# Optimization experiments

Hardware: AMD Instinct MI355X
Metric: run time of the kernel (lower is better)

The kernel has to match this reference:

```python
import jax, jax.numpy as jnp
import numpy as np

HEADS = 4
DIM_HEAD = 32
SCALE = DIM_HEAD ** (-0.5)


def setup_inputs() -> dict:
    key = jax.random.key(0)
    k0, k1, k2 = jax.random.split(key, 3)
    B, C, H, W = 4, 256, 64, 64
    inner = HEADS * DIM_HEAD  # 128
    x = jax.random.normal(k0, (B, C, H, W), dtype=jnp.float32)
    # 1x1 conv weights reduce to matrices (out_ch, in_ch)
    w_qkv = jax.random.normal(k1, (3 * inner, C), dtype=jnp.float32) * 0.02
    w_out = jax.random.normal(k2, (C, inner), dtype=jnp.float32) * 0.02
    b_out = jnp.zeros((C,), dtype=jnp.float32)
    return {"x": x, "w_qkv": w_qkv, "w_out": w_out, "b_out": b_out}


def reference(x, w_qkv, w_out, b_out):
    b, c, h, w = x.shape
    n = h * w  # flattened spatial length
    inner = HEADS * DIM_HEAD
    # 1x1 conv == channel matmul: [b, 3*inner, h, w]
    qkv = jnp.einsum('oc,bchw->bohw', w_qkv, x)
    qkv = qkv.reshape(b, 3, HEADS, DIM_HEAD, n)  # split 3 * (heads dim_head)
    q, k, v = qkv[:, 0], qkv[:, 1], qkv[:, 2]    # each [b, heads, d, n]
    sim = jnp.einsum('bhdi,bhdj->bhij', q * SCALE, k)  # [b, h, n, n]
    attn = jax.nn.softmax(sim, axis=-1)  # stable (max-subtract) softmax
    out = jnp.einsum('bhij,bhdj->bhid', attn, v)       # [b, heads, n, d]
    # 'b h (x y) d -> b (h d) x y'
    out = out.transpose(0, 1, 3, 2).reshape(b, inner, h, w)
    y = jnp.einsum('oc,bchw->bohw', w_out, out) + b_out[None, :, None, None]
    return y
```

## Files before the change

kernel.cpp:

```cpp
#include <hip/hip_runtime.h>

#define N_TOK 4096
#define BATCH 4

typedef __attribute__((ext_vector_type(8))) short short8;
typedef __attribute__((ext_vector_type(4))) float floatx4;

__device__ __forceinline__ unsigned pack_rnd(float a, float b) {
    unsigned ra = __float_as_uint(a) + 0x8000u;
    unsigned rb = __float_as_uint(b) + 0x8000u;
    return __builtin_amdgcn_perm(rb, ra, 0x07060302u);
}

__device__ __forceinline__ void split_pack(float a, float b,
                                           unsigned &ph, unsigned &pl) {
    unsigned ra = __float_as_uint(a) + 0x8000u;
    unsigned rb = __float_as_uint(b) + 0x8000u;
    ph = __builtin_amdgcn_perm(rb, ra, 0x07060302u);
    float la = a - __uint_as_float(ra & 0xffff0000u);
    float lb = b - __uint_as_float(rb & 0xffff0000u);
    pl = __builtin_amdgcn_perm(__float_as_uint(lb) + 0x8000u,
                               __float_as_uint(la) + 0x8000u, 0x07060302u);
}

__device__ __forceinline__ short8 mk_short8(unsigned p0, unsigned p1,
                                            unsigned p2, unsigned p3) {
    union { unsigned u[4]; short8 s; } c;
    c.u[0] = p0; c.u[1] = p1; c.u[2] = p2; c.u[3] = p3;
    return c.s;
}

__device__ __forceinline__ void cvt_frag(const float* src,
                                         short8 &hi, short8 &lo) {
    float4 w0 = *(const float4*)src;
    float4 w1 = *(const float4*)(src + 4);
    unsigned ph[4], pl[4];
    split_pack(w0.x, w0.y, ph[0], pl[0]);
    split_pack(w0.z, w0.w, ph[1], pl[1]);
    split_pack(w1.x, w1.y, ph[2], pl[2]);
    split_pack(w1.z, w1.w, ph[3], pl[3]);
    hi = mk_short8(ph[0], ph[1], ph[2], ph[3]);
    lo = mk_short8(pl[0], pl[1], pl[2], pl[3]);
}

__device__ __forceinline__ float fast_exp2(float x) {
#if __has_builtin(__builtin_amdgcn_exp2f)
    return __builtin_amdgcn_exp2f(x);
#else
    return exp2f(x);
#endif
}

__global__ __launch_bounds__(256) void gemm1_fused(
    const float* __restrict__ wq, const float* __restrict__ x,
    unsigned short* __restrict__ Qp, unsigned short* __restrict__ Kp,
    unsigned short* __restrict__ Vp)
{
    const int N = N_TOK;
    const int b = blockIdx.z;
    const int row0 = blockIdx.y * 64;
    const int col0 = blockIdx.x * 64;
    const int t = threadIdx.x;
    const int wave = t >> 6, lane = t & 63;
    const int l16 = lane & 15, quad = lane >> 4;
    const int msub0 = (wave & 1) * 32, nsub0 = (wave >> 1) * 32;

    __shared__ __align__(16) char smem[29184];
    float (*Xf)[68] = (float(*)[68])smem;
    unsigned short* XsH = (unsigned short*)(smem + 8704);
    unsigned short* XsL = (unsigned short*)(smem + 13824);
    unsigned short* WsH = (unsigned short*)(smem + 18944);
    unsigned short* WsL = (unsigned short*)(smem + 24064);

    floatx4 acc[2][2] = {};

    const int xr = t >> 3, xnb = (t & 7) * 8;
    const int tnr = t >> 2, tkb = (t & 3) * 8;
    const int wm = t >> 2, wk = (t & 3) * 8;

    for (int kc = 0; kc < 8; ++kc) {
        __syncthreads();
        {
            const float* wsrc = wq + (size_t)(row0 + wm) * 256 + kc * 32 + wk;
            float4 w0 = *(const float4*)wsrc;
            float4 w1 = *(const float4*)(wsrc + 4);
            unsigned ph[4], pl[4];
            split_pack(w0.x, w0.y, ph[0], pl[0]);
            split_pack(w0.z, w0.w, ph[1], pl[1]);
            split_pack(w1.x, w1.y, ph[2], pl[2]);
            split_pack(w1.z, w1.w, ph[3], pl[3]);
            *(uint4*)(WsH + wm * 40 + wk) = *(uint4*)ph;
            *(uint4*)(WsL + wm * 40 + wk) = *(uint4*)pl;
        }
        {
            const float* src = x + ((size_t)b * 256 + kc * 32 + xr) * N + col0 + xnb;
            *(float4*)&Xf[xr][xnb]     = *(const float4*)src;
            *(float4*)&Xf[xr][xnb + 4] = *(const float4*)(src + 4);
        }
        __syncthreads();
        {
            unsigned ph[4], pl[4];
#pragma unroll
            for (int q = 0; q < 4; ++q)
                split_pack(Xf[tkb + 2 * q][tnr], Xf[tkb + 2 * q + 1][tnr],
                           ph[q], pl[q]);
            *(uint4*)(XsH + tnr * 40 + tkb) = *(uint4*)ph;
            *(uint4*)(XsL + tnr * 40 + tkb) = *(uint4*)pl;
        }
        __syncthreads();
        short8 ah0 = *(const short8*)(WsH + (msub0 + l16) * 40 + quad * 8);
        short8 ah1 = *(const short8*)(WsH + (msub0 + 16 + l16) * 40 + quad * 8);
        short8 al0 = *(const short8*)(WsL + (msub0 + l16) * 40 + quad * 8);
        short8 al1 = *(const short8*)(WsL + (msub0 + 16 + l16) * 40 + quad * 8);
        short8 bh0 = *(const short8*)(XsH + (nsub0 + l16) * 40 + quad * 8);
        short8 bh1 = *(const short8*)(XsH + (nsub0 + 16 + l16) * 40 + quad * 8);
        short8 bl0 = *(const short8*)(XsL + (nsub0 + l16) * 40 + quad * 8);
        short8 bl1 = *(const short8*)(XsL + (nsub0 + 16 + l16) * 40 + quad * 8);
        acc[0][0] = __builtin_amdgcn_mfma_f32_16x16x32_bf16(ah0, bh0, acc[0][0], 0, 0, 0);
        acc[0][1] = __builtin_amdgcn_mfma_f32_16x16x32_bf16(ah0, bh1, acc[0][1], 0, 0, 0);
        acc[1][0] = __builtin_amdgcn_mfma_f32_16x16x32_bf16(ah1, bh0, acc[1][0], 0, 0, 0);
        acc[1][1] = __builtin_amdgcn_mfma_f32_16x16x32_bf16(ah1, bh1, acc[1][1], 0, 0, 0);
        acc[0][0] = __builtin_amdgcn_mfma_f32_16x16x32_bf16(ah0, bl0, acc[0][0], 0, 0, 0);
        acc[0][1] = __builtin_amdgcn_mfma_f32_16x16x32_bf16(ah0, bl1, acc[0][1], 0, 0, 0);
        acc[1][0] = __builtin_amdgcn_mfma_f32_16x16x32_bf16(ah1, bl0, acc[1][0], 0, 0, 0);
        acc[1][1] = __builtin_amdgcn_mfma_f32_16x16x32_bf16(ah1, bl1, acc[1][1], 0, 0, 0);
        acc[0][0] = __builtin_amdgcn_mfma_f32_16x16x32_bf16(al0, bh0, acc[0][0], 0, 0, 0);
        acc[0][1] = __builtin_amdgcn_mfma_f32_16x16x32_bf16(al0, bh1, acc[0][1], 0, 0, 0);
        acc[1][0] = __builtin_amdgcn_mfma_f32_16x16x32_bf16(al1, bh0, acc[1][0], 0, 0, 0);
        acc[1][1] = __builtin_amdgcn_mfma_f32_16x16x32_bf16(al1, bh1, acc[1][1], 0, 0, 0);
    }

    __syncthreads();
    const int region = row0 >> 7;
    if (region == 2) {
        float (*LdsF)[68] = (float(*)[68])smem;
#pragma unroll
        for (int i = 0; i < 2; ++i)
#pragma unroll
            for (int j = 0; j < 2; ++j) {
                const int m = msub0 + i * 16 + quad * 4;
                const int n = nsub0 + j * 16 + l16;
#pragma unroll
                for (int r = 0; r < 4; ++r) LdsF[m + r][n] = acc[i][j][r];
            }
        __syncthreads();
        const int m = t >> 2, nb2 = (t & 3) * 16;
        const int vrow = b * 128 + (row0 - 256) + m;
        unsigned pk[8];
#pragma unroll
        for (int q = 0; q < 8; ++q)
            pk[q] = pack_rnd(LdsF[m][nb2 + 2 * q], LdsF[m][nb2 + 2 * q + 1]);
        unsigned short* dst = Vp + (size_t)vrow * N + col0 + nb2;
        *(uint4*)&dst[0] = *(uint4*)&pk[0];
        *(uint4*)&dst[8] = *(uint4*)&pk[4];
    } else {
        unsigned short (*LdsT)[68] = (unsigned short(*)[68])smem;
        const float sc = region ? 1.0f
                                : (0.17677669529663687f * 1.4426950408889634f);
#pragma unroll
        for (int i = 0; i < 2; ++i)
#pragma unroll
            for (int j = 0; j < 2; ++j) {
                const int m = msub0 + i * 16 + quad * 4;
                const int n = nsub0 + j * 16 + l16;
                uint2 pr;
                pr.x = pack_rnd(acc[i][j][0] * sc, acc[i][j][1] * sc);
                pr.y = pack_rnd(acc[i][j][2] * sc, acc[i][j][3] * sc);
                *(uint2*)&LdsT[n][m] = pr;
            }
        __syncthreads();
        const int n = t & 63, hb = (t >> 6) & 1, dh = t >> 7;
        const int h = ((row0 & 127) >> 5) + hb;
        const int m0 = hb * 32 + dh * 16;
        unsigned tmp[8];
        *(uint2*)&tmp[0] = *(const uint2*)&LdsT[n][m0];
        *(uint2*)&tmp[2] = *(const uint2*)&LdsT[n][m0 + 4];
        *(uint2*)&tmp[4] = *(const uint2*)&LdsT[n][m0 + 8];
        *(uint2*)&tmp[6] = *(const uint2*)&LdsT[n][m0 + 12];
        unsigned short* dst = (region ? Kp : Qp) +
            ((size_t)(b * 4 + h) * N + col0 + n) * 32 + dh * 16;
        *(uint4*)&dst[0] = *(uint4*)&tmp[0];
        *(uint4*)&dst[8] = *(uint4*)&tmp[4];
    }
}

__global__ __launch_bounds__(512) void attn_fused(
    const unsigned short* __restrict__ Qp,
    const unsigned short* __restrict__ Kp,
    const unsigned short* __restrict__ Vp,
    unsigned short* __restrict__ Oth, unsigned short* __restrict__ Otl)
{
    const int N = N_TOK;
    const int bh = blockIdx.y;
    const int b = bh >> 2, h = bh & 3;
    const int i0 = blockIdx.x * 128;
    const int t = threadIdx.x;
    const int wave = t >> 6, lane = t & 63;
    const int l16 = lane & 15, quad = lane >> 4;
    const int team = wave >> 2, w4 = wave & 3;

    __shared__ __align__(16) char smem[75776];
    unsigned short* S = (unsigned short*)smem;
    unsigned short* PtW = S + 19456 + wave * 2304;

    short8 ones;
#pragma unroll
    for (int e = 0; e < 8; ++e) ones[e] = (short)0x3F80;

    short8 qh[2];
#pragma unroll
    for (int g = 0; g < 2; ++g)
        qh[g] = *(const short8*)(Qp +
            ((size_t)bh * N + i0 + w4 * 32 + g * 16 + l16) * 32 + quad * 8);

    floatx4 o[2][2] = {};
    floatx4 lacc[2] = {};

    const int st_k = t & 255;
    const int skey = st_k >> 2, sdp = (st_k & 3) * 8;
    const int svd = st_k >> 3, svp = (st_k & 7) * 8;
    const unsigned short* kp0 = Kp + ((size_t)bh * N + skey) * 32 + sdp;
    const unsigned short* kp1 = kp0 + (size_t)2048 * 32;
    const unsigned short* vp0 = Vp + ((size_t)bh * 32 + svd) * N + svp;
    const unsigned short* vp1 = vp0 + 2048;

    short8 r0, r1;
    if (t < 256) { r0 = *(const short8*)kp0; r1 = *(const short8*)kp1; }
    else         { r0 = *(const short8*)vp0; r1 = *(const short8*)vp1; }
    if (t < 256) {
        *(short8*)(S + skey * 40 + sdp) = r0;
        *(short8*)(S + 2560 + skey * 40 + sdp) = r1;
    } else {
        *(short8*)(S + 10240 + svd * 72 + svp) = r0;
        *(short8*)(S + 10240 + 2304 + svd * 72 + svp) = r1;
    }
    kp0 += 64 * 32; kp1 += 64 * 32; vp0 += 64; vp1 += 64;
    if (t < 256) { r0 = *(const short8*)kp0; r1 = *(const short8*)kp1; }
    else         { r0 = *(const short8*)vp0; r1 = *(const short8*)vp1; }
    __syncthreads();

    for (int it = 0; it < 32; ++it) {
        const int cur = it & 1;
        if (it + 1 < 32) {
            const int nb = 1 - cur;
            if (t < 256) {
                *(short8*)(S + nb * 5120 + skey * 40 + sdp) = r0;
                *(short8*)(S + nb * 5120 + 2560 + skey * 40 + sdp) = r1;
            } else {
                *(short8*)(S + 10240 + nb * 4608 + svd * 72 + svp) = r0;
                *(short8*)(S + 10240 + nb * 4608 + 2304 + svd * 72 + svp) = r1;
            }
        }
        if (it + 2 < 32) {
            kp0 += 64 * 32; kp1 += 64 * 32; vp0 += 64; vp1 += 64;
            if (t < 256) { r0 = *(const short8*)kp0; r1 = *(const short8*)kp1; }
            else         { r0 = *(const short8*)vp0; r1 = *(const short8*)vp1; }
        }

        const unsigned short* Ksr = S + cur * 5120 + team * 2560;
        const unsigned short* Vsr = S + 10240 + cur * 4608 + team * 2304;

        short8 kh0 = *(const short8*)(Ksr + ( 0 + l16) * 40 + quad * 8);
        short8 kh1 = *(const short8*)(Ksr + (16 + l16) * 40 + quad * 8);
        short8 kh2 = *(const short8*)(Ksr + (32 + l16) * 40 + quad * 8);
        short8 kh3 = *(const short8*)(Ksr + (48 + l16) * 40 + quad * 8);

#pragma unroll
        for (int g = 0; g < 2; ++g) {
            const floatx4 z = {0.0f, 0.0f, 0.0f, 0.0f};
            floatx4 stv[4];
            stv[0] = __builtin_amdgcn_mfma_f32_16x16x32_bf16(kh0, qh[g], z, 0, 0, 0);
            stv[1] = __builtin_amdgcn_mfma_f32_16x16x32_bf16(kh1, qh[g], z, 0, 0, 0);
            stv[2] = __builtin_amdgcn_mfma_f32_16x16x32_bf16(kh2, qh[g], z, 0, 0, 0);
            stv[3] = __builtin_amdgcn_mfma_f32_16x16x32_bf16(kh3, qh[g], z, 0, 0, 0);
#pragma unroll
            for (int s = 0; s < 4; ++s) {
                float p0 = fast_exp2(stv[s][0]);
                float p1 = fast_exp2(stv[s][1]);
                float p2 = fast_exp2(stv[s][2]);
                float p3 = fast_exp2(stv[s][3]);
                uint2 pr;
                pr.x = pack_rnd(p0, p1);
                pr.y = pack_rnd(p2, p3);
                *(uint2*)(PtW + (g * 16 + l16) * 72 + s * 16 + quad * 4) = pr;
            }
        }

#pragma unroll
        for (int ks = 0; ks < 2; ++ks) {
            short8 pf0 = *(const short8*)(PtW + ( 0 + l16) * 72 + ks * 32 + quad * 8);
            short8 pf1 = *(const short8*)(PtW + (16 + l16) * 72 + ks * 32 + quad * 8);
            short8 vh0 = *(const short8*)(Vsr + ( 0 + l16) * 72 + ks * 32 + quad * 8);
            short8 vh1 = *(const short8*)(Vsr + (16 + l16) * 72 + ks * 32 + quad * 8);
            o[0][0] = __builtin_amdgcn_mfma_f32_16x16x32_bf16(vh0, pf0, o[0][0], 0, 0, 0);
            o[0][1] = __builtin_amdgcn_mfma_f32_16x16x32_bf16(vh1, pf0, o[0][1], 0, 0, 0);
            o[1][0] = __builtin_amdgcn_mfma_f32_16x16x32_bf16(vh0, pf1, o[1][0], 0, 0, 0);
            o[1][1] = __builtin_amdgcn_mfma_f32_16x16x32_bf16(vh1, pf1, o[1][1], 0, 0, 0);
            lacc[0] = __builtin_amdgcn_mfma_f32_16x16x32_bf16(ones, pf0, lacc[0], 0, 0, 0);
            lacc[1] = __builtin_amdgcn_mfma_f32_16x16x32_bf16(ones, pf1, lacc[1], 0, 0, 0);
        }
        __syncthreads();
    }

    float (*OfB)[132] = (float(*)[132])smem;
    float* Lb = (float*)(smem + 16896);
    float (*OfA)[132] = (float(*)[132])(smem + 17408);

    if (team == 1) {
#pragma unroll
        for (int g = 0; g < 2; ++g) {
            const int q = w4 * 32 + g * 16 + l16;
#pragma unroll
            for (int half = 0; half < 2; ++half)
#pragma unroll
                for (int r = 0; r < 4; ++r)
                    OfB[half * 16 + quad * 4 + r][q] = o[g][half][r];
            if (quad == 0) Lb[q] = lacc[g][0];
        }
    }
    __syncthreads();
    if (team == 0) {
#pragma unroll
        for (int g = 0; g < 2; ++g) {
            const int q = w4 * 32 + g * 16 + l16;
            const float inv = 1.0f / (lacc[g][0] + Lb[q]);
#pragma unroll
            for (int half = 0; half < 2; ++half)
#pragma unroll
                for (int r = 0; r < 4; ++r) {
                    const int d = half * 16 + quad * 4 + r;
                    OfA[d][q] = (o[g][half][r] + OfB[d][q]) * inv;
                }
        }
    }
    __syncthreads();
    {
        const int q = t >> 2, db = (t & 3) * 8;
        unsigned ph[4], pl[4];
#pragma unroll
        for (int i = 0; i < 4; ++i)
            split_pack(OfA[db + 2 * i][q], OfA[db + 2 * i + 1][q], ph[i], pl[i]);
        const size_t off = ((size_t)b * N + i0 + q) * 128 + h * 32 + db;
        *(uint4*)(Oth + off) = *(uint4*)ph;
        *(uint4*)(Otl + off) = *(uint4*)pl;
    }
}

__global__ __launch_bounds__(256) void gemm2_fused(
    const float* __restrict__ wo,
    const unsigned short* __restrict__ Oth, const unsigned short* __restrict__ Otl,
    const float* __restrict__ bias, float* __restrict__ y)
{
    const int N = N_TOK;
    const int b = blockIdx.z;
    const int row0 = blockIdx.y * 64;
    const int col0 = blockIdx.x * 64;
    const int t = threadIdx.x;
    const int wave = t >> 6, lane = t & 63;
    const int l16 = lane & 15, quad = lane >> 4;
    const int msub0 = (wave & 1) * 32, nsub0 = (wave >> 1) * 32;

    __shared__ __align__(16) char smem[17408];
    unsigned short* BsH = (unsigned short*)smem;
    unsigned short* BsL = (unsigned short*)(smem + 5120);
    float (*LdsF)[68] = (float(*)[68])smem;

    short8 ah[4][2], al[4][2];
#pragma unroll
    for (int kc = 0; kc < 4; ++kc)
#pragma unroll
        for (int r = 0; r < 2; ++r)
            cvt_frag(wo + (size_t)(row0 + msub0 + r * 16 + l16) * 128 +
                         kc * 32 + quad * 8,
                     ah[kc][r], al[kc][r]);

    const int srow = t >> 2, sk = (t & 3) * 8;
    const unsigned short* gH = Oth + ((size_t)b * N + col0 + srow) * 128 + sk;
    const unsigned short* gL = Otl + ((size_t)b * N + col0 + srow) * 128 + sk;

    floatx4 acc[2][2] = {};
#pragma unroll
    for (int kc = 0; kc < 4; ++kc) {
        short8 hreg = *(const short8*)(gH + kc * 32);
        short8 lreg = *(const short8*)(gL + kc * 32);
        __syncthreads();
        *(short8*)(BsH + srow * 40 + sk) = hreg;
        *(short8*)(BsL + srow * 40 + sk) = lreg;
        __syncthreads();
        short8 bh0 = *(const short8*)(BsH + (nsub0 + l16) * 40 + quad * 8);
        short8 bh1 = *(const short8*)(BsH + (nsub0 + 16 + l16) * 40 + quad * 8);
        short8 bl0 = *(const short8*)(BsL + (nsub0 + l16) * 40 + quad * 8);
        short8 bl1 = *(const short8*)(BsL + (nsub0 + 16 + l16) * 40 + quad * 8);
        acc[0][0] = __builtin_amdgcn_mfma_f32_16x16x32_bf16(ah[kc][0], bh0, acc[0][0], 0, 0, 0);
        acc[0][1] = __builtin_amdgcn_mfma_f32_16x16x32_bf16(ah[kc][0], bh1, acc[0][1], 0, 0, 0);
        acc[1][0] = __builtin_amdgcn_mfma_f32_16x16x32_bf16(ah[kc][1], bh0, acc[1][0], 0, 0, 0);
        acc[1][1] = __builtin_amdgcn_mfma_f32_16x16x32_bf16(ah[kc][1], bh1, acc[1][1], 0, 0, 0);
        acc[0][0] = __builtin_amdgcn_mfma_f32_16x16x32_bf16(ah[kc][0], bl0, acc[0][0], 0, 0, 0);
        acc[0][1] = __builtin_amdgcn_mfma_f32_16x16x32_bf16(ah[kc][0], bl1, acc[0][1], 0, 0, 0);
        acc[1][0] = __builtin_amdgcn_mfma_f32_16x16x32_bf16(ah[kc][1], bl0, acc[1][0], 0, 0, 0);
        acc[1][1] = __builtin_amdgcn_mfma_f32_16x16x32_bf16(ah[kc][1], bl1, acc[1][1], 0, 0, 0);
        acc[0][0] = __builtin_amdgcn_mfma_f32_16x16x32_bf16(al[kc][0], bh0, acc[0][0], 0, 0, 0);
        acc[0][1] = __builtin_amdgcn_mfma_f32_16x16x32_bf16(al[kc][0], bh1, acc[0][1], 0, 0, 0);
        acc[1][0] = __builtin_amdgcn_mfma_f32_16x16x32_bf16(al[kc][1], bh0, acc[1][0], 0, 0, 0);
        acc[1][1] = __builtin_amdgcn_mfma_f32_16x16x32_bf16(al[kc][1], bh1, acc[1][1], 0, 0, 0);
    }

    __syncthreads();
#pragma unroll
    for (int i = 0; i < 2; ++i)
#pragma unroll
        for (int j = 0; j < 2; ++j) {
            const int m = msub0 + i * 16 + quad * 4;
            const int n = nsub0 + j * 16 + l16;
#pragma unroll
            for (int r = 0; r < 4; ++r) LdsF[m + r][n] = acc[i][j][r];
        }
    __syncthreads();
    const int m = t >> 2, nb = (t & 3) * 16;
    const float bv = bias[row0 + m];
    float* dst = y + ((size_t)b * 256 + row0 + m) * N + col0 + nb;
#pragma unroll
    for (int g = 0; g < 4; ++g) {
        float4 o4;
        o4.x = LdsF[m][nb + g * 4 + 0] + bv;
        o4.y = LdsF[m][nb + g * 4 + 1] + bv;
        o4.z = LdsF[m][nb + g * 4 + 2] + bv;
        o4.w = LdsF[m][nb + g * 4 + 3] + bv;
        *(float4*)(dst + g * 4) = o4;
    }
}

extern "C" void kernel_launch(void* const* d_in, const int* in_sizes, int n_in,
                              void* d_out, int out_size, void* d_ws, size_t ws_size,
                              hipStream_t stream) {
    const float* x     = (const float*)d_in[0];
    const float* w_qkv = (const float*)d_in[1];
    const float* w_out = (const float*)d_in[2];
    const float* b_out = (const float*)d_in[3];
    float* y = (float*)d_out;

    char* base = (char*)d_ws;
    unsigned short* Qp  = (unsigned short*)base;
    unsigned short* Kp  = Qp + (size_t)16 * N_TOK * 32;
    unsigned short* Vp  = Kp + (size_t)16 * N_TOK * 32;
    unsigned short* Oth = Vp + (size_t)16 * N_TOK * 32;
    unsigned short* Otl = Oth + (size_t)BATCH * N_TOK * 128;

    gemm1_fused<<<dim3(64, 6, BATCH), dim3(256), 0, stream>>>(
        w_qkv, x, Qp, Kp, Vp);
    attn_fused<<<dim3(32, 16), dim3(512), 0, stream>>>(Qp, Kp, Vp, Oth, Otl);
    gemm2_fused<<<dim3(64, 4, BATCH), dim3(256), 0, stream>>>(
        w_out, Oth, Otl, b_out, y);
}
```

Before: 168.0 us.

## Keep softmax probabilities in registers by permuting K rows in shared memory

Permutes the shared-memory slot order of staged K rows so the S-matrix MFMA output layout matches the B-operand layout needed by the PV MFMA. The exponentiated probabilities are then packed straight into registers instead of going through a per-wave LDS round trip. This removes the per-wave P buffer, roughly halves shared memory use and raises the occupancy hint to 6 blocks. The risks are more register pressure and a permutation that must exactly match the MFMA lane layout.

```diff
diff --git a/kernel.cpp b/kernel.cpp
--- a/kernel.cpp
+++ b/kernel.cpp
@@ -184,7 +184,7 @@
     }
 }
 
-__global__ __launch_bounds__(512) void attn_fused(
+__global__ __launch_bounds__(512, 6) void attn_fused(
     const unsigned short* __restrict__ Qp,
     const unsigned short* __restrict__ Kp,
     const unsigned short* __restrict__ Vp,
@@ -199,9 +199,8 @@
     const int l16 = lane & 15, quad = lane >> 4;
     const int team = wave >> 2, w4 = wave & 3;
 
-    __shared__ __align__(16) char smem[75776];
+    __shared__ __align__(16) char smem[38912];
     unsigned short* S = (unsigned short*)smem;
-    unsigned short* PtW = S + 19456 + wave * 2304;
 
     short8 ones;
 #pragma unroll
@@ -218,6 +217,8 @@
 
     const int st_k = t & 255;
     const int skey = st_k >> 2, sdp = (st_k & 3) * 8;
+    const int sslot = (skey & 32) | ((skey & 4) << 2) | ((skey & 24) >> 1)
+                    | (skey & 3);
     const int svd = st_k >> 3, svp = (st_k & 7) * 8;
     const unsigned short* kp0 = Kp + ((size_t)bh * N + skey) * 32 + sdp;
     const unsigned short* kp1 = kp0 + (size_t)2048 * 32;
@@ -228,8 +229,8 @@
     if (t < 256) { r0 = *(const short8*)kp0; r1 = *(const short8*)kp1; }
     else         { r0 = *(const short8*)vp0; r1 = *(const short8*)vp1; }
     if (t < 256) {
-        *(short8*)(S + skey * 40 + sdp) = r0;
-        *(short8*)(S + 2560 + skey * 40 + sdp) = r1;
+        *(short8*)(S + sslot * 40 + sdp) = r0;
+        *(short8*)(S + 2560 + sslot * 40 + sdp) = r1;
     } else {
         *(short8*)(S + 10240 + svd * 72 + svp) = r0;
         *(short8*)(S + 10240 + 2304 + svd * 72 + svp) = r1;
@@ -244,8 +245,8 @@
         if (it + 1 < 32) {
             const int nb = 1 - cur;
             if (t < 256) {
-                *(short8*)(S + nb * 5120 + skey * 40 + sdp) = r0;
-                *(short8*)(S + nb * 5120 + 2560 + skey * 40 + sdp) = r1;
+                *(short8*)(S + nb * 5120 + sslot * 40 + sdp) = r0;
+                *(short8*)(S + nb * 5120 + 2560 + sslot * 40 + sdp) = r1;
             } else {
                 *(short8*)(S + 10240 + nb * 4608 + svd * 72 + svp) = r0;
                 *(short8*)(S + 10240 + nb * 4608 + 2304 + svd * 72 + svp) = r1;
@@ -264,40 +265,34 @@
         short8 kh1 = *(const short8*)(Ksr + (16 + l16) * 40 + quad * 8);
         short8 kh2 = *(const short8*)(Ksr + (32 + l16) * 40 + quad * 8);
         short8 kh3 = *(const short8*)(Ksr + (48 + l16) * 40 + quad * 8);
+        short8 vh00 = *(const short8*)(Vsr + ( 0 + l16) * 72 +  0 + quad * 8);
+        short8 vh01 = *(const short8*)(Vsr + (16 + l16) * 72 +  0 + quad * 8);
+        short8 vh10 = *(const short8*)(Vsr + ( 0 + l16) * 72 + 32 + quad * 8);
+        short8 vh11 = *(const short8*)(Vsr + (16 + l16) * 72 + 32 + quad * 8);
 
 #pragma unroll
         for (int g = 0; g < 2; ++g) {
             const floatx4 z = {0.0f, 0.0f, 0.0f, 0.0f};
-            floatx4 stv[4];
-            stv[0] = __builtin_amdgcn_mfma_f32_16x16x32_bf16(kh0, qh[g], z, 0, 0, 0);
-            stv[1] = __builtin_amdgcn_mfma_f32_16x16x32_bf16(kh1, qh[g], z, 0, 0, 0);
-            stv[2] = __builtin_amdgcn_mfma_f32_16x16x32_bf16(kh2, qh[g], z, 0, 0, 0);
-            stv[3] = __builtin_amdgcn_mfma_f32_16x16x32_bf16(kh3, qh[g], z, 0, 0, 0);
-#pragma unroll
-            for (int s = 0; s < 4; ++s) {
-                float p0 = fast_exp2(stv[s][0]);
-                float p1 = fast_exp2(stv[s][1]);
-                float p2 = fast_exp2(stv[s][2]);
-                float p3 = fast_exp2(stv[s][3]);
-                uint2 pr;
-                pr.x = pack_rnd(p0, p1);
-                pr.y = pack_rnd(p2, p3);
-                *(uint2*)(PtW + (g * 16 + l16) * 72 + s * 16 + quad * 4) = pr;
-            }
-        }
-
-#pragma unroll
-        for (int ks = 0; ks < 2; ++ks) {
-            short8 pf0 = *(const short8*)(PtW + ( 0 + l16) * 72 + ks * 32 + quad * 8);
-            short8 pf1 = *(const short8*)(PtW + (16 + l16) * 72 + ks * 32 + quad * 8);
-            short8 vh0 = *(const short8*)(Vsr + ( 0 + l16) * 72 + ks * 32 + quad * 8);
-            short8 vh1 = *(const short8*)(Vsr + (16 + l16) * 72 + ks * 32 + quad * 8);
-            o[0][0] = __builtin_amdgcn_mfma_f32_16x16x32_bf16(vh0, pf0, o[0][0], 0, 0, 0);
-            o[0][1] = __builtin_amdgcn_mfma_f32_16x16x32_bf16(vh1, pf0, o[0][1], 0, 0, 0);
-            o[1][0] = __builtin_amdgcn_mfma_f32_16x16x32_bf16(vh0, pf1, o[1][0], 0, 0, 0);
-            o[1][1] = __builtin_amdgcn_mfma_f32_16x16x32_bf16(vh1, pf1, o[1][1], 0, 0, 0);
-            lacc[0] = __builtin_amdgcn_mfma_f32_16x16x32_bf16(ones, pf0, lacc[0], 0, 0, 0);
-            lacc[1] = __builtin_amdgcn_mfma_f32_16x16x32_bf16(ones, pf1, lacc[1], 0, 0, 0);
+            floatx4 s0 = __builtin_amdgcn_mfma_f32_16x16x32_bf16(kh0, qh[g], z, 0, 0, 0);
+            floatx4 s1 = __builtin_amdgcn_mfma_f32_16x16x32_bf16(kh1, qh[g], z, 0, 0, 0);
+            floatx4 s2 = __builtin_amdgcn_mfma_f32_16x16x32_bf16(kh2, qh[g], z, 0, 0, 0);
+            floatx4 s3 = __builtin_amdgcn_mfma_f32_16x16x32_bf16(kh3, qh[g], z, 0, 0, 0);
+            short8 pf0 = mk_short8(
+                pack_rnd(fast_exp2(s0[0]), fast_exp2(s0[1])),
+                pack_rnd(fast_exp2(s0[2]), fast_exp2(s0[3])),
+                pack_rnd(fast_exp2(s1[0]), fast_exp2(s1[1])),
+                pack_rnd(fast_exp2(s1[2]), fast_exp2(s1[3])));
+            o[g][0] = __builtin_amdgcn_mfma_f32_16x16x32_bf16(vh00, pf0, o[g][0], 0, 0, 0);
+            o[g][1] = __builtin_amdgcn_mfma_f32_16x16x32_bf16(vh01, pf0, o[g][1], 0, 0, 0);
+            lacc[g] = __builtin_amdgcn_mfma_f32_16x16x32_bf16(ones, pf0, lacc[g], 0, 0, 0);
+            short8 pf1 = mk_short8(
+                pack_rnd(fast_exp2(s2[0]), fast_exp2(s2[1])),
+                pack_rnd(fast_exp2(s2[2]), fast_exp2(s2[3])),
+                pack_rnd(fast_exp2(s3[0]), fast_exp2(s3[1])),
+                pack_rnd(fast_exp2(s3[2]), fast_exp2(s3[3])));
+            o[g][0] = __builtin_amdgcn_mfma_f32_16x16x32_bf16(vh10, pf1, o[g][0], 0, 0, 0);
+            o[g][1] = __builtin_amdgcn_mfma_f32_16x16x32_bf16(vh11, pf1, o[g][1], 0, 0, 0);
+            lacc[g] = __builtin_amdgcn_mfma_f32_16x16x32_bf16(ones, pf1, lacc[g], 0, 0, 0);
         }
         __syncthreads();
     }
```

After: 217.3 us. +29.3%, slower.
